# Kernel tuning notes

Hardware: AMD Instinct MI355X
Metric: run time of the kernel (lower is better)

Reference implementation:

```python
import jax, jax.numpy as jnp
import numpy as np

N, E, P, IN, H = 1024, 65536, 1024, 128, 64
LN_EPS = 1e-5


def _layernorm(x, g, b):
    mu = x.mean(-1, keepdims=True)
    var = ((x - mu) ** 2).mean(-1, keepdims=True)
    return (x - mu) * jax.lax.rsqrt(var + LN_EPS) * g + b


def _gcn(x, ei, W, b, n):
    # PyG GCNConv: out = D^{-1/2} (A + I) D^{-1/2} X W + b
    row, col = ei[0], ei[1]
    xw = x @ W
    deg = jnp.zeros((n,), xw.dtype).at[col].add(1.0) + 1.0  # self-loop adds 1
    dinv = jax.lax.rsqrt(deg)
    coef = (dinv[row] * dinv[col])[:, None]
    out = jnp.zeros_like(xw).at[col].add(xw[row] * coef)
    out = out + xw * (dinv * dinv)[:, None]  # self-loop message
    return out + b


def setup_inputs() -> dict:
    key = jax.random.key(0)
    ks = jax.random.split(key, 20)
    f32 = jnp.float32
    inp = {
        "x": jax.random.normal(ks[0], (N, IN), f32),
        "ei": jax.random.randint(ks[1], (2, E), 0, N, dtype=jnp.int32),
        "pos": jax.random.randint(ks[2], (2, P), 0, N, dtype=jnp.int32),
        # GCNConv(input, hidden) and GCNConv(hidden, hidden)
        "W_g1": jax.random.normal(ks[3], (IN, H), f32) * (IN ** -0.5),
        "b_g1": jnp.zeros((H,), f32),
        "W_g2": jax.random.normal(ks[4], (H, H), f32) * (H ** -0.5),
        "b_g2": jnp.zeros((H,), f32),
        # mlp1: Linear + LayerNorm (+Dropout eval=id) + ReLU
        "W_m1": jax.random.normal(ks[5], (H, H), f32) * (H ** -0.5),
        "b_m1": jnp.zeros((H,), f32),
        "g_m1": jnp.ones((H,), f32),
        "be_m1": jnp.zeros((H,), f32),
        # mlp2
        "W_m2": jax.random.normal(ks[6], (H, H), f32) * (H ** -0.5),
        "b_m2": jnp.zeros((H,), f32),
        "g_m2": jnp.ones((H,), f32),
        "be_m2": jnp.zeros((H,), f32),
        # mlp3: Linear(2H,H) + ReLU + Linear(H,1)
        "W_a": jax.random.normal(ks[7], (2 * H, H), f32) * ((2 * H) ** -0.5),
        "b_a": jnp.zeros((H,), f32),
        "W_b": jax.random.normal(ks[8], (H, 1), f32) * (H ** -0.5),
        "b_b": jnp.zeros((1,), f32),
    }
    return inp


def reference(x, ei, pos, W_g1, b_g1, W_g2, b_g2, W_m1, b_m1, g_m1, be_m1,
              W_m2, b_m2, g_m2, be_m2, W_a, b_a, W_b, b_b):
    n = x.shape[0]
    # forward_routine
    h = _gcn(x, ei, W_g1, b_g1, n)
    h = _gcn(h, ei, W_g2, b_g2, n)
    xx = h[pos[0]] * h[pos[1]]          # [P, H] pairwise node products at queries
    xe = h[ei[0]] * h[ei[1]]            # [E, H] pairwise node products at edges
    x1 = jax.nn.relu(_layernorm(xe @ W_m1 + b_m1, g_m1, be_m1))  # mlp1
    x2 = jax.nn.relu(_layernorm(xe @ W_m2 + b_m2, g_m2, be_m2))  # mlp2
    # dense_bmm / sparse_bmm followed by combine() keeps only entries at pos
    # pairs, so compute res[pos0, pos1, :] = sum_k D1[pos0, k, :] * D2[k, pos1, :]
    D1 = jnp.zeros((n, n, H), x2.dtype).at[ei[0], ei[1]].set(x2)  # mlp2 output: left operand
    D2 = jnp.zeros((n, n, H), x1.dtype).at[ei[0], ei[1]].set(x1)  # mlp1 output: right operand
    r1 = D1[pos[0]]                                   # [P, N, H]
    c2 = jnp.swapaxes(jnp.take(D2, pos[1], axis=1), 0, 1)  # [P, N, H]
    pos_val = jnp.einsum('pnh,pnh->ph', r1, c2)       # [P, H]
    feat = jnp.concatenate([pos_val, xx], axis=1)     # combine -> [P, 2H]
    hid = jax.nn.relu(feat @ W_a + b_a)               # mlp3 (dropout = identity at eval)
    return (hid @ W_b + b_b).squeeze(-1)              # [P]
```

## Files before the change

kernel.cpp:

```cpp
#include <hip/hip_runtime.h>

#define Nn 1024
#define Ee 65536
#define Pq 1024
#define CAP 160

typedef unsigned long long ull;

__global__ __launch_bounds__(256) void k_zero(uint4* __restrict__ z) {
    z[blockIdx.x * 256 + threadIdx.x] = make_uint4(0, 0, 0, 0);
}

__global__ __launch_bounds__(256) void k_front(const float* __restrict__ x,
                                               const float* __restrict__ Wg1,
                                               float* __restrict__ xw1,
                                               const int* __restrict__ ei,
                                               int* __restrict__ degI,
                                               int* __restrict__ adj,
                                               ull* __restrict__ Mbit,
                                               ull* __restrict__ MTbit) {
    __shared__ float sW[8192];
    int tid = threadIdx.x;
    int gid = blockIdx.x * 256 + tid;
    for (int i = tid; i < 2048; i += 256)
        ((float4*)sW)[i] = ((const float4*)Wg1)[i];
    __syncthreads();
    {
        int lane = gid & 63;
        int r = __builtin_amdgcn_readfirstlane(gid >> 6);
        const float* xr = x + r * 128;
        float acc = 0.f;
        #pragma unroll 8
        for (int j = 0; j < 128; ++j) acc = fmaf(xr[j], sW[j * 64 + lane], acc);
        xw1[gid] = acc;
    }
    {
        int r = ei[gid], c = ei[Ee + gid];
        int slot = atomicAdd(&degI[c], 1);
        if (slot < CAP) adj[c * CAP + slot] = r;
        atomicOr(&Mbit[r * 16 + (c >> 6)], 1ull << (c & 63));
        atomicOr(&MTbit[c * 16 + (r >> 6)], 1ull << (r & 63));
    }
}

__device__ __forceinline__ float gather_quarter(const int* __restrict__ adj,
                                                const float* __restrict__ xwsrc,
                                                const float* s_dinv, int c, int w,
                                                int n, int lane) {
    const int* al = adj + c * CAP;
    float acc = 0.f;
    int j = w, end = n;
    for (; j + 28 < end; j += 32) {
        int r0 = al[j],      r1 = al[j + 4],  r2 = al[j + 8],  r3 = al[j + 12];
        int r4 = al[j + 16], r5 = al[j + 20], r6 = al[j + 24], r7 = al[j + 28];
        float a0 = xwsrc[r0 * 64 + lane] * s_dinv[r0];
        float a1 = xwsrc[r1 * 64 + lane] * s_dinv[r1];
        float a2 = xwsrc[r2 * 64 + lane] * s_dinv[r2];
        float a3 = xwsrc[r3 * 64 + lane] * s_dinv[r3];
        float a4 = xwsrc[r4 * 64 + lane] * s_dinv[r4];
        float a5 = xwsrc[r5 * 64 + lane] * s_dinv[r5];
        float a6 = xwsrc[r6 * 64 + lane] * s_dinv[r6];
        float a7 = xwsrc[r7 * 64 + lane] * s_dinv[r7];
        acc += ((a0 + a1) + (a2 + a3)) + ((a4 + a5) + (a6 + a7));
    }
    for (; j < end; j += 4) {
        int r = al[j];
        acc += xwsrc[r * 64 + lane] * s_dinv[r];
    }
    return acc;
}

__global__ __launch_bounds__(256) void k_gather1(const int* __restrict__ adj,
                                                 const int* __restrict__ degI,
                                                 const float* __restrict__ xw1,
                                                 const float* __restrict__ Wg2,
                                                 const float* __restrict__ bg1,
                                                 float* __restrict__ xw2) {
    __shared__ float sW[4096];
    __shared__ float s_dinv[Nn];
    __shared__ float red[4][64];
    int tid = threadIdx.x;
    int lane = tid & 63;
    int w = tid >> 6;
    int c = blockIdx.x;
    for (int i = tid; i < 1024; i += 256)
        ((float4*)sW)[i] = ((const float4*)Wg2)[i];
    {
        int4 d4 = ((const int4*)degI)[tid];
        s_dinv[4 * tid]     = rsqrtf((float)d4.x + 1.f);
        s_dinv[4 * tid + 1] = rsqrtf((float)d4.y + 1.f);
        s_dinv[4 * tid + 2] = rsqrtf((float)d4.z + 1.f);
        s_dinv[4 * tid + 3] = rsqrtf((float)d4.w + 1.f);
    }
    __syncthreads();
    int n = __builtin_amdgcn_readfirstlane(degI[c]);
    if (n > CAP) n = CAP;
    float acc = gather_quarter(adj, xw1, s_dinv, c, w, n, lane);
    red[w][lane] = acc;
    __syncthreads();
    if (w == 0) {
        float a = (red[0][lane] + red[1][lane]) + (red[2][lane] + red[3][lane]);
        float dc = s_dinv[c];
        float h1c = dc * a + dc * dc * xw1[c * 64 + lane] + bg1[lane];
        float t = 0.f;
        #pragma unroll 8
        for (int j = 0; j < 64; ++j) t = fmaf(__shfl(h1c, j), sW[j * 64 + lane], t);
        xw2[c * 64 + lane] = t;
    }
}

__global__ __launch_bounds__(256) void k_gather2(const int* __restrict__ adj,
                                                 const int* __restrict__ degI,
                                                 const float* __restrict__ xw2,
                                                 const float* __restrict__ bg2,
                                                 float* __restrict__ h2) {
    __shared__ float s_dinv[Nn];
    __shared__ float red[4][64];
    int tid = threadIdx.x;
    int lane = tid & 63;
    int w = tid >> 6;
    int c = blockIdx.x;
    {
        int4 d4 = ((const int4*)degI)[tid];
        s_dinv[4 * tid]     = rsqrtf((float)d4.x + 1.f);
        s_dinv[4 * tid + 1] = rsqrtf((float)d4.y + 1.f);
        s_dinv[4 * tid + 2] = rsqrtf((float)d4.z + 1.f);
        s_dinv[4 * tid + 3] = rsqrtf((float)d4.w + 1.f);
    }
    __syncthreads();
    int n = __builtin_amdgcn_readfirstlane(degI[c]);
    if (n > CAP) n = CAP;
    float acc = gather_quarter(adj, xw2, s_dinv, c, w, n, lane);
    red[w][lane] = acc;
    __syncthreads();
    if (w == 0) {
        float a = (red[0][lane] + red[1][lane]) + (red[2][lane] + red[3][lane]);
        float dc = s_dinv[c];
        h2[c * 64 + lane] = dc * a + dc * dc * xw2[c * 64 + lane] + bg2[lane];
    }
}

__global__ __launch_bounds__(256) void k_posfinal(
    const int* __restrict__ pos,
    const ull* __restrict__ Mbit, const ull* __restrict__ MTbit,
    const float* __restrict__ h2,
    const float* __restrict__ W1, const float* __restrict__ b1,
    const float* __restrict__ g1, const float* __restrict__ be1,
    const float* __restrict__ W2, const float* __restrict__ b2,
    const float* __restrict__ g2, const float* __restrict__ be2,
    const float* __restrict__ Wa, const float* __restrict__ ba,
    const float* __restrict__ Wb, const float* __restrict__ bb,
    float* __restrict__ out) {
    __shared__ float W1s[4096], W2s[4096];
    __shared__ float s_red[2][64];
    int tid = threadIdx.x;
    for (int i = tid; i < 1024; i += 256) {
        ((float4*)W1s)[i] = ((const float4*)W1)[i];
        ((float4*)W2s)[i] = ((const float4*)W2)[i];
    }
    __syncthreads();
    int lane = tid & 63;
    int wv = tid >> 6;
    int q = wv >> 1;
    int half = wv & 1;
    int p = blockIdx.x * 2 + q;
    int a = __builtin_amdgcn_readfirstlane(pos[p]);
    int b = __builtin_amdgcn_readfirstlane(pos[Pq + p]);
    float ha = h2[a * 64 + lane], hb = h2[b * 64 + lane];
    float lb1 = b1[lane], lg1 = g1[lane], lbe1 = be1[lane];
    float lb2 = b2[lane], lg2 = g2[lane], lbe2 = be2[lane];
    float acc = 0.f;
    for (int wd = half; wd < 16; wd += 2) {
        ull bits = Mbit[a * 16 + wd] & MTbit[b * 16 + wd];
        while (bits) {
            int k = (wd << 6) + __ffsll(bits) - 1;
            bits &= bits - 1;
            float hk = h2[k * 64 + lane];
            float xeA = ha * hk;
            float xeB = hk * hb;
            float a2 = lb2, a1 = lb1;
            #pragma unroll 8
            for (int j = 0; j < 64; ++j) {
                float vA = __shfl(xeA, j);
                float vB = __shfl(xeB, j);
                a2 = fmaf(vA, W2s[j * 64 + lane], a2);
                a1 = fmaf(vB, W1s[j * 64 + lane], a1);
            }
            float s2 = a2, q2 = a2 * a2, s1 = a1, q1 = a1 * a1;
            for (int off = 32; off; off >>= 1) {
                s2 += __shfl_xor(s2, off); q2 += __shfl_xor(q2, off);
                s1 += __shfl_xor(s1, off); q1 += __shfl_xor(q1, off);
            }
            float mu2 = s2 * (1.f / 64.f), mu1 = s1 * (1.f / 64.f);
            float v2 = q2 * (1.f / 64.f) - mu2 * mu2;
            float v1 = q1 * (1.f / 64.f) - mu1 * mu1;
            float r2v = rsqrtf(v2 + 1e-5f), r1v = rsqrtf(v1 + 1e-5f);
            float x2v = fmaxf(0.f, (a2 - mu2) * r2v * lg2 + lbe2);
            float x1v = fmaxf(0.f, (a1 - mu1) * r1v * lg1 + lbe1);
            acc += x2v * x1v;
        }
    }
    if (half) s_red[q][lane] = acc;
    __syncthreads();
    if (!half) {
        acc += s_red[q][lane];
        float xx = ha * hb;
        float t = ba[lane];
        #pragma unroll 8
        for (int j = 0; j < 64; ++j) {
            t = fmaf(__shfl(acc, j), Wa[j * 64 + lane], t);
            t = fmaf(__shfl(xx, j), Wa[(64 + j) * 64 + lane], t);
        }
        t = fmaxf(t, 0.f);
        float v = t * Wb[lane];
        for (int off = 32; off; off >>= 1) v += __shfl_xor(v, off);
        if (lane == 0) out[p] = v + bb[0];
    }
}

extern "C" void kernel_launch(void* const* d_in, const int* in_sizes, int n_in,
                              void* d_out, int out_size, void* d_ws, size_t ws_size,
                              hipStream_t stream) {
    const float* x    = (const float*)d_in[0];
    const int*   ei   = (const int*)d_in[1];
    const int*   pos  = (const int*)d_in[2];
    const float* Wg1  = (const float*)d_in[3];
    const float* bg1  = (const float*)d_in[4];
    const float* Wg2  = (const float*)d_in[5];
    const float* bg2  = (const float*)d_in[6];
    const float* Wm1  = (const float*)d_in[7];
    const float* bm1  = (const float*)d_in[8];
    const float* gm1  = (const float*)d_in[9];
    const float* bem1 = (const float*)d_in[10];
    const float* Wm2  = (const float*)d_in[11];
    const float* bm2  = (const float*)d_in[12];
    const float* gm2  = (const float*)d_in[13];
    const float* bem2 = (const float*)d_in[14];
    const float* Wa   = (const float*)d_in[15];
    const float* ba   = (const float*)d_in[16];
    const float* Wb   = (const float*)d_in[17];
    const float* bb   = (const float*)d_in[18];
    float* out = (float*)d_out;

    char* w = (char*)d_ws;
    char* zbase = w;
    int* degI = (int*)w;  w += 1024 * 4;
    ull* Mbit = (ull*)w;  w += 1024 * 16 * 8;
    ull* MTbit = (ull*)w; w += 1024 * 16 * 8;
    int*   adj = (int*)w;   w += (size_t)Nn * CAP * 4;
    float* xw1 = (float*)w; w += 65536 * 4;
    float* xw2 = (float*)w; w += 65536 * 4;
    float* h2  = (float*)w; w += 65536 * 4;

    k_zero<<<65, 256, 0, stream>>>((uint4*)zbase);
    k_front<<<256, 256, 0, stream>>>(x, Wg1, xw1, ei, degI, adj, Mbit, MTbit);
    k_gather1<<<Nn, 256, 0, stream>>>(adj, degI, xw1, Wg2, bg1, xw2);
    k_gather2<<<Nn, 256, 0, stream>>>(adj, degI, xw2, bg2, h2);
    k_posfinal<<<Pq / 2, 256, 0, stream>>>(pos, Mbit, MTbit, h2,
                                           Wm1, bm1, gm1, bem1,
                                           Wm2, bm2, gm2, bem2,
                                           Wa, ba, Wb, bb, out);
}
```

Before: 65.07 us.

## Split front kernel blocks, stage adjacency in LDS, spread pos pairs over four waves

The front kernel now runs 512 blocks, half doing the x@W matmul and half doing the edge scatter/bitmask atomics, so the atomic work no longer waits behind the weight load and sync. The gather kernels copy each node's adjacency list into shared memory once instead of every wave reading it from global memory. The pos kernel gives each query pair a whole block and splits the 16 bitmask words over four waves instead of two, reducing the per-wave serial intersection work. The cost is more blocks, each reloading the MLP weights into LDS, and an extra shared reduction.

```diff
diff --git a/kernel.cpp b/kernel.cpp
--- a/kernel.cpp
+++ b/kernel.cpp
@@ -21,11 +21,12 @@
                                                ull* __restrict__ MTbit) {
     __shared__ float sW[8192];
     int tid = threadIdx.x;
-    int gid = blockIdx.x * 256 + tid;
-    for (int i = tid; i < 2048; i += 256)
-        ((float4*)sW)[i] = ((const float4*)Wg1)[i];
-    __syncthreads();
-    {
+    int B = blockIdx.x;
+    if (B < 256) {
+        int gid = B * 256 + tid;
+        for (int i = tid; i < 2048; i += 256)
+            ((float4*)sW)[i] = ((const float4*)Wg1)[i];
+        __syncthreads();
         int lane = gid & 63;
         int r = __builtin_amdgcn_readfirstlane(gid >> 6);
         const float* xr = x + r * 128;
@@ -33,9 +34,9 @@
         #pragma unroll 8
         for (int j = 0; j < 128; ++j) acc = fmaf(xr[j], sW[j * 64 + lane], acc);
         xw1[gid] = acc;
-    }
-    {
-        int r = ei[gid], c = ei[Ee + gid];
+    } else {
+        int e = (B - 256) * 256 + tid;
+        int r = ei[e], c = ei[Ee + e];
         int slot = atomicAdd(&degI[c], 1);
         if (slot < CAP) adj[c * CAP + slot] = r;
         atomicOr(&Mbit[r * 16 + (c >> 6)], 1ull << (c & 63));
@@ -43,16 +44,15 @@
     }
 }
 
-__device__ __forceinline__ float gather_quarter(const int* __restrict__ adj,
+__device__ __forceinline__ float gather_quarter(const int* __restrict__ s_adj,
                                                 const float* __restrict__ xwsrc,
-                                                const float* s_dinv, int c, int w,
+                                                const float* s_dinv, int w,
                                                 int n, int lane) {
-    const int* al = adj + c * CAP;
     float acc = 0.f;
     int j = w, end = n;
     for (; j + 28 < end; j += 32) {
-        int r0 = al[j],      r1 = al[j + 4],  r2 = al[j + 8],  r3 = al[j + 12];
-        int r4 = al[j + 16], r5 = al[j + 20], r6 = al[j + 24], r7 = al[j + 28];
+        int r0 = s_adj[j],      r1 = s_adj[j + 4],  r2 = s_adj[j + 8],  r3 = s_adj[j + 12];
+        int r4 = s_adj[j + 16], r5 = s_adj[j + 20], r6 = s_adj[j + 24], r7 = s_adj[j + 28];
         float a0 = xwsrc[r0 * 64 + lane] * s_dinv[r0];
         float a1 = xwsrc[r1 * 64 + lane] * s_dinv[r1];
         float a2 = xwsrc[r2 * 64 + lane] * s_dinv[r2];
@@ -64,7 +64,7 @@
         acc += ((a0 + a1) + (a2 + a3)) + ((a4 + a5) + (a6 + a7));
     }
     for (; j < end; j += 4) {
-        int r = al[j];
+        int r = s_adj[j];
         acc += xwsrc[r * 64 + lane] * s_dinv[r];
     }
     return acc;
@@ -78,6 +78,7 @@
                                                  float* __restrict__ xw2) {
     __shared__ float sW[4096];
     __shared__ float s_dinv[Nn];
+    __shared__ int s_adj[CAP];
     __shared__ float red[4][64];
     int tid = threadIdx.x;
     int lane = tid & 63;
@@ -92,10 +93,11 @@
         s_dinv[4 * tid + 2] = rsqrtf((float)d4.z + 1.f);
         s_dinv[4 * tid + 3] = rsqrtf((float)d4.w + 1.f);
     }
-    __syncthreads();
     int n = __builtin_amdgcn_readfirstlane(degI[c]);
     if (n > CAP) n = CAP;
-    float acc = gather_quarter(adj, xw1, s_dinv, c, w, n, lane);
+    if (tid < n) s_adj[tid] = adj[c * CAP + tid];
+    __syncthreads();
+    float acc = gather_quarter(s_adj, xw1, s_dinv, w, n, lane);
     red[w][lane] = acc;
     __syncthreads();
     if (w == 0) {
@@ -115,6 +117,7 @@
                                                  const float* __restrict__ bg2,
                                                  float* __restrict__ h2) {
     __shared__ float s_dinv[Nn];
+    __shared__ int s_adj[CAP];
     __shared__ float red[4][64];
     int tid = threadIdx.x;
     int lane = tid & 63;
@@ -127,10 +130,11 @@
         s_dinv[4 * tid + 2] = rsqrtf((float)d4.z + 1.f);
         s_dinv[4 * tid + 3] = rsqrtf((float)d4.w + 1.f);
     }
-    __syncthreads();
     int n = __builtin_amdgcn_readfirstlane(degI[c]);
     if (n > CAP) n = CAP;
-    float acc = gather_quarter(adj, xw2, s_dinv, c, w, n, lane);
+    if (tid < n) s_adj[tid] = adj[c * CAP + tid];
+    __syncthreads();
+    float acc = gather_quarter(s_adj, xw2, s_dinv, w, n, lane);
     red[w][lane] = acc;
     __syncthreads();
     if (w == 0) {
@@ -152,7 +156,7 @@
     const float* __restrict__ Wb, const float* __restrict__ bb,
     float* __restrict__ out) {
     __shared__ float W1s[4096], W2s[4096];
-    __shared__ float s_red[2][64];
+    __shared__ float s_red[3][64];
     int tid = threadIdx.x;
     for (int i = tid; i < 1024; i += 256) {
         ((float4*)W1s)[i] = ((const float4*)W1)[i];
@@ -161,16 +165,14 @@
     __syncthreads();
     int lane = tid & 63;
     int wv = tid >> 6;
-    int q = wv >> 1;
-    int half = wv & 1;
-    int p = blockIdx.x * 2 + q;
+    int p = blockIdx.x;
     int a = __builtin_amdgcn_readfirstlane(pos[p]);
     int b = __builtin_amdgcn_readfirstlane(pos[Pq + p]);
     float ha = h2[a * 64 + lane], hb = h2[b * 64 + lane];
     float lb1 = b1[lane], lg1 = g1[lane], lbe1 = be1[lane];
     float lb2 = b2[lane], lg2 = g2[lane], lbe2 = be2[lane];
     float acc = 0.f;
-    for (int wd = half; wd < 16; wd += 2) {
+    for (int wd = wv; wd < 16; wd += 4) {
         ull bits = Mbit[a * 16 + wd] & MTbit[b * 16 + wd];
         while (bits) {
             int k = (wd << 6) + __ffsll(bits) - 1;
@@ -200,10 +202,10 @@
             acc += x2v * x1v;
         }
     }
-    if (half) s_red[q][lane] = acc;
-    __syncthreads();
-    if (!half) {
-        acc += s_red[q][lane];
+    if (wv) s_red[wv - 1][lane] = acc;
+    __syncthreads();
+    if (wv == 0) {
+        acc += (s_red[0][lane] + s_red[1][lane]) + s_red[2][lane];
         float xx = ha * hb;
         float t = ba[lane];
         #pragma unroll 8
@@ -253,11 +255,11 @@
     float* h2  = (float*)w; w += 65536 * 4;
 
     k_zero<<<65, 256, 0, stream>>>((uint4*)zbase);
-    k_front<<<256, 256, 0, stream>>>(x, Wg1, xw1, ei, degI, adj, Mbit, MTbit);
+    k_front<<<512, 256, 0, stream>>>(x, Wg1, xw1, ei, degI, adj, Mbit, MTbit);
     k_gather1<<<Nn, 256, 0, stream>>>(adj, degI, xw1, Wg2, bg1, xw2);
     k_gather2<<<Nn, 256, 0, stream>>>(adj, degI, xw2, bg2, h2);
-    k_posfinal<<<Pq / 2, 256, 0, stream>>>(pos, Mbit, MTbit, h2,
-                                           Wm1, bm1, gm1, bem1,
-                                           Wm2, bm2, gm2, bem2,
-                                           Wa, ba, Wb, bb, out);
-}
+    k_posfinal<<<Pq, 256, 0, stream>>>(pos, Mbit, MTbit, h2,
+                                       Wm1, bm1, gm1, bem1,
+                                       Wm2, bm2, gm2, bem2,
+                                       Wa, ba, Wb, bb, out);
+}
```

Result: faster. 63.77 us (median of 2 runs) (-2.0%).
